# Kernel optimization log

Measured on AMD Instinct MI355X. Metric: run time of the kernel, lower is better.

## Reference

```python
import jax, jax.numpy as jnp
import numpy as np

THRESH_POSITIVE_AFFINITY = 0.65
THRESH_POSITIVE_REGION = 0.6
LAMBDA_WEIGHT = 2.0
TOPK_FALLBACK = 500


def _single_image_loss(pre_loss, label, thresh_positive):
    """Vectorized version of the per-sample pos/neg split + hard-negative top-k.

    pre_loss, label: [B, N] (flattened per-sample masked MSE maps / GT maps).
    Returns scalar sum over the batch of (pos_loss + neg_loss) per sample.
    """
    B, N = pre_loss.shape
    pos_mask = label > thresh_positive                      # [B, N] bool
    n_pos = jnp.sum(pos_mask, axis=-1)                      # [B] int
    n_neg = N - n_pos                                       # [B] int

    # positive loss: mean over positive pixels (0 if none)
    pos_sum = jnp.sum(jnp.where(pos_mask, pre_loss, 0.0), axis=-1)
    pos_loss = jnp.where(n_pos > 0, pos_sum / jnp.maximum(n_pos, 1), 0.0)

    # negatives sorted descending; positives pushed to the end via -inf
    neg_vals = jnp.where(pos_mask, -jnp.inf, pre_loss)
    sorted_neg = -jnp.sort(-neg_vals, axis=-1)              # [B, N] descending
    sorted_neg = jnp.where(jnp.isfinite(sorted_neg), sorted_neg, 0.0)
    csum = jnp.cumsum(sorted_neg, axis=-1)                  # [B, N]

    # k = 3*n_pos if enough negatives, else all negatives (torch branch)
    k = jnp.minimum(3 * n_pos, n_neg)                       # [B]
    k_idx = jnp.maximum(k - 1, 0)
    topk_sum = jnp.take_along_axis(csum, k_idx[:, None], axis=-1)[:, 0]
    neg_loss = jnp.where(k > 0, topk_sum / jnp.maximum(k, 1), 0.0)

    # fallback when no positives: mean of global top-500 of the loss map
    top500 = jnp.mean(jax.lax.top_k(pre_loss, TOPK_FALLBACK)[0], axis=-1)

    per_sample = jnp.where(n_pos > 0, pos_loss + neg_loss, top500)
    return jnp.sum(per_sample)


def setup_inputs() -> dict:
    key = jax.random.key(0)
    k1, k2, k3, k4, k5 = jax.random.split(key, 5)
    shape = (32, 512, 512)
    return {
        "region_score_gt": jax.random.uniform(k1, shape, dtype=jnp.float32),
        "affinity_score_gt": jax.random.uniform(k2, shape, dtype=jnp.float32),
        "region_score_pred": jax.random.normal(k3, shape, dtype=jnp.float32),
        "affinity_score_pred": jax.random.normal(k4, shape, dtype=jnp.float32),
        "mask": jax.random.uniform(k5, shape, dtype=jnp.float32),
    }


def reference(region_score_gt, affinity_score_gt, region_score_pred,
              affinity_score_pred, mask):
    # clamp predictions to 1 where GT is positive and pred overshoots 1
    rp = jnp.where((region_score_gt > THRESH_POSITIVE_REGION)
                   & (region_score_pred > 1.0), 1.0, region_score_pred)
    ap = jnp.where((affinity_score_gt > THRESH_POSITIVE_AFFINITY)
                   & (affinity_score_pred > 1.0), 1.0, affinity_score_pred)

    loss_g = (rp - region_score_gt) ** 2 * mask             # masked MSE map
    loss_a = (ap - affinity_score_gt) ** 2 * mask

    B = loss_g.shape[0]
    char_loss = _single_image_loss(loss_g.reshape(B, -1),
                                   region_score_gt.reshape(B, -1),
                                   THRESH_POSITIVE_REGION)
    affi_loss = _single_image_loss(loss_a.reshape(B, -1),
                                   affinity_score_gt.reshape(B, -1),
                                   THRESH_POSITIVE_AFFINITY)
    return LAMBDA_WEIGHT * char_loss / B + affi_loss / B
```

## Files before the change

kernel.cpp:

```cpp
#include <hip/hip_runtime.h>


#define NPS (512 * 512)
#define BPS 64
#define EPB 4096
#define NB 32

constexpr float THR_REGION = 0.6f;
constexpr float THR_AFF    = 0.65f;

__global__ __launch_bounds__(256) void map_loss_pass1(
    const float* __restrict__ rg, const float* __restrict__ ag,
    const float* __restrict__ rp, const float* __restrict__ ap,
    const float* __restrict__ mk, float* __restrict__ part) {
  const int b   = blockIdx.y;
  const int tid = threadIdx.x;
  const size_t sbase = (size_t)b * NPS + (size_t)blockIdx.x * EPB;

  float v[6] = {0.f, 0.f, 0.f, 0.f, 0.f, 0.f};

#pragma unroll
  for (int jj = 0; jj < 4; ++jj) {
    const size_t base = sbase + (size_t)jj * 1024 + (size_t)tid * 4;
    const float4 g_r = *reinterpret_cast<const float4*>(rg + base);
    const float4 g_a = *reinterpret_cast<const float4*>(ag + base);
    const float4 p_r = *reinterpret_cast<const float4*>(rp + base);
    const float4 p_a = *reinterpret_cast<const float4*>(ap + base);
    const float4 m_4 = *reinterpret_cast<const float4*>(mk + base);
    const float* gr = reinterpret_cast<const float*>(&g_r);
    const float* ga = reinterpret_cast<const float*>(&g_a);
    const float* pr = reinterpret_cast<const float*>(&p_r);
    const float* pa = reinterpret_cast<const float*>(&p_a);
    const float* mm = reinterpret_cast<const float*>(&m_4);
#pragma unroll
    for (int j = 0; j < 4; ++j) {
      const float m = mm[j];
      {
        const float g = gr[j];
        float p = pr[j];
        const bool pos = g > THR_REGION;
        if (pos && p > 1.0f) p = 1.0f;
        const float d = p - g;
        const float l = d * d * m;
        if (pos) { v[0] += l; v[2] += 1.0f; } else { v[1] += l; }
      }
      {
        const float g = ga[j];
        float p = pa[j];
        const bool pos = g > THR_AFF;
        if (pos && p > 1.0f) p = 1.0f;
        const float d = p - g;
        const float l = d * d * m;
        if (pos) { v[3] += l; v[5] += 1.0f; } else { v[4] += l; }
      }
    }
  }

#pragma unroll
  for (int q = 0; q < 6; ++q)
#pragma unroll
    for (int off = 32; off > 0; off >>= 1)
      v[q] += __shfl_down(v[q], off, 64);

  __shared__ float sh[4][6];
  const int lane = tid & 63, wid = tid >> 6;
  if (lane == 0) {
#pragma unroll
    for (int q = 0; q < 6; ++q) sh[wid][q] = v[q];
  }
  __syncthreads();
  if (tid < 6) {
    const float s = sh[0][tid] + sh[1][tid] + sh[2][tid] + sh[3][tid];
    part[((size_t)b * BPS + blockIdx.x) * 6 + tid] = s;
  }
}

__device__ float topk_sum_row(const float* __restrict__ gt,
                              const float* __restrict__ pd,
                              const float* __restrict__ mm,
                              float thr, int k, bool negOnly) {
  unsigned prefix = 0;
  float sum_def = 0.f;
  int want = k;
  for (int shift = 24; shift >= 0; shift -= 8) {
    unsigned cnt[256];
    float bsum[256];
    for (int i = 0; i < 256; ++i) { cnt[i] = 0; bsum[i] = 0.f; }
    for (int j = 0; j < NPS; ++j) {
      const float g = gt[j];
      const bool pos = g > thr;
      if (negOnly && pos) continue;
      float p = pd[j];
      if (pos && p > 1.0f) p = 1.0f;
      const float d = p - g;
      const float vv = d * d * mm[j];
      const unsigned u = __float_as_uint(vv);
      if (shift < 24 && (u >> (shift + 8)) != (prefix >> (shift + 8))) continue;
      const unsigned bin = (u >> shift) & 255u;
      cnt[bin]++;
      bsum[bin] += vv;
    }
    int bin = 255;
    for (; bin > 0; --bin) {
      if ((int)cnt[bin] < want) { want -= (int)cnt[bin]; sum_def += bsum[bin]; }
      else break;
    }
    prefix |= ((unsigned)bin) << shift;
  }
  sum_def += (float)want * __uint_as_float(prefix);
  return sum_def;
}

__global__ __launch_bounds__(64) void map_loss_pass2(
    const float* __restrict__ part,
    const float* __restrict__ rg, const float* __restrict__ ag,
    const float* __restrict__ rp, const float* __restrict__ ap,
    const float* __restrict__ mk, float* __restrict__ out) {
  const int t = threadIdx.x;
  const int mapA = t >> 5;
  const int b = t & 31;

  float posSum = 0.f, negSum = 0.f, cntF = 0.f;
  for (int blk = 0; blk < BPS; ++blk) {
    const float* p = part + ((size_t)b * BPS + blk) * 6 + mapA * 3;
    posSum += p[0];
    negSum += p[1];
    cntF   += p[2];
  }

  const int npos = (int)cntF;
  const int nneg = NPS - npos;
  long long k = 3LL * npos;
  if (k > nneg) k = nneg;

  const float thr = mapA ? THR_AFF : THR_REGION;
  const float* gt = (mapA ? ag : rg) + (size_t)b * NPS;
  const float* pd = (mapA ? ap : rp) + (size_t)b * NPS;
  const float* mm = mk + (size_t)b * NPS;

  float per_sample;
  if (npos > 0) {
    const float pos_loss = posSum / (float)npos;
    float neg_loss = 0.f;
    if (k > 0) {
      if (k == (long long)nneg) {
        neg_loss = negSum / (float)nneg;
      } else {
        neg_loss = topk_sum_row(gt, pd, mm, thr, (int)k, true) / (float)k;
      }
    }
    per_sample = pos_loss + neg_loss;
  } else {
    per_sample = topk_sum_row(gt, pd, mm, thr, 500, false) / 500.0f;
  }

  __shared__ float sh[64];
  sh[t] = per_sample;
  __syncthreads();
  if (t == 0) {
    float char_sum = 0.f, affi_sum = 0.f;
    for (int i = 0; i < 32; ++i) { char_sum += sh[i]; affi_sum += sh[32 + i]; }
    out[0] = 2.0f * char_sum / (float)NB + affi_sum / (float)NB;
  }
}

extern "C" void kernel_launch(void* const* d_in, const int* in_sizes, int n_in,
                              void* d_out, int out_size, void* d_ws, size_t ws_size,
                              hipStream_t stream) {
  const float* rg = (const float*)d_in[0];
  const float* ag = (const float*)d_in[1];
  const float* rp = (const float*)d_in[2];
  const float* ap = (const float*)d_in[3];
  const float* mk = (const float*)d_in[4];
  float* out = (float*)d_out;
  float* part = (float*)d_ws;

  dim3 grid1(BPS, NB);
  map_loss_pass1<<<grid1, 256, 0, stream>>>(rg, ag, rp, ap, mk, part);
  map_loss_pass2<<<1, 64, 0, stream>>>(part, rg, ag, rp, ap, mk, out);
}
```

Before: 34.47 us.

## Fuse partial reduction and finalization via last-block counter with cooperative top-k

Merges the two kernels into one: each block writes its partial sums, bumps an atomic counter, and the last block to finish does the per-sample finalization. The single-thread radix top-k is replaced by a 256-thread cooperative radix select using shared-memory histograms. This removes the separate tiny second kernel and its serial work, at the cost of an extra memset launch and atomic/threadfence overhead.

Result: slower. 106.2 us (+208.1%).

```diff
diff --git a/kernel.cpp b/kernel.cpp
--- a/kernel.cpp
+++ b/kernel.cpp
@@ -5,14 +5,81 @@
 #define BPS 64
 #define EPB 4096
 #define NB 32
+#define NBLK (BPS * NB)
 
 constexpr float THR_REGION = 0.6f;
 constexpr float THR_AFF    = 0.65f;
 
-__global__ __launch_bounds__(256) void map_loss_pass1(
+__device__ float coop_topk_sum(const float* __restrict__ gt,
+                               const float* __restrict__ pd,
+                               const float* __restrict__ mm,
+                               float thr, int k, bool negOnly, int tid) {
+  __shared__ unsigned hcnt[256];
+  __shared__ unsigned s_prefix;
+  __shared__ int s_want;
+  if (tid == 0) { s_prefix = 0; s_want = k; }
+  __syncthreads();
+  for (int shift = 24; shift >= 0; shift -= 8) {
+    hcnt[tid] = 0;
+    __syncthreads();
+    const unsigned pfx = s_prefix;
+    for (int j = tid; j < NPS; j += 256) {
+      const float g = gt[j];
+      const bool pos = g > thr;
+      if (negOnly && pos) continue;
+      float p = pd[j];
+      if (pos && p > 1.0f) p = 1.0f;
+      const float d = p - g;
+      const float vv = d * d * mm[j];
+      const unsigned u = __float_as_uint(vv);
+      if (shift < 24 && (u >> (shift + 8)) != (pfx >> (shift + 8))) continue;
+      atomicAdd(&hcnt[(u >> shift) & 255u], 1u);
+    }
+    __syncthreads();
+    if (tid == 0) {
+      int want = s_want;
+      int bin = 255;
+      for (; bin > 0; --bin) {
+        if ((int)hcnt[bin] < want) want -= (int)hcnt[bin];
+        else break;
+      }
+      s_want = want;
+      s_prefix |= ((unsigned)bin) << shift;
+    }
+    __syncthreads();
+  }
+  const unsigned T = s_prefix;
+  const int ties = s_want;
+  float psum = 0.f;
+  for (int j = tid; j < NPS; j += 256) {
+    const float g = gt[j];
+    const bool pos = g > thr;
+    if (negOnly && pos) continue;
+    float p = pd[j];
+    if (pos && p > 1.0f) p = 1.0f;
+    const float d = p - g;
+    const float vv = d * d * mm[j];
+    if (__float_as_uint(vv) > T) psum += vv;
+  }
+#pragma unroll
+  for (int off = 32; off; off >>= 1) psum += __shfl_down(psum, off, 64);
+  __shared__ float wsum[4];
+  if ((tid & 63) == 0) wsum[tid >> 6] = psum;
+  __syncthreads();
+  float total = 0.f;
+  if (tid == 0)
+    total = ((wsum[0] + wsum[1]) + (wsum[2] + wsum[3])) +
+            (float)ties * __uint_as_float(T);
+  __syncthreads();
+  return total;
+}
+
+__global__ __launch_bounds__(256) void map_loss_fused(
     const float* __restrict__ rg, const float* __restrict__ ag,
     const float* __restrict__ rp, const float* __restrict__ ap,
-    const float* __restrict__ mk, float* __restrict__ part) {
+    const float* __restrict__ mk,
+    unsigned* __restrict__ counter, float* __restrict__ part,
+    float* __restrict__ out) {
   const int b   = blockIdx.y;
   const int tid = threadIdx.x;
   const size_t sbase = (size_t)b * NPS + (size_t)blockIdx.x * EPB;
@@ -62,105 +129,93 @@
     for (int off = 32; off > 0; off >>= 1)
       v[q] += __shfl_down(v[q], off, 64);
 
-  __shared__ float sh[4][6];
+  __shared__ float shW[4][6];
   const int lane = tid & 63, wid = tid >> 6;
   if (lane == 0) {
 #pragma unroll
-    for (int q = 0; q < 6; ++q) sh[wid][q] = v[q];
-  }
-  __syncthreads();
-  if (tid < 6) {
-    const float s = sh[0][tid] + sh[1][tid] + sh[2][tid] + sh[3][tid];
-    part[((size_t)b * BPS + blockIdx.x) * 6 + tid] = s;
-  }
-}
-
-__device__ float topk_sum_row(const float* __restrict__ gt,
-                              const float* __restrict__ pd,
-                              const float* __restrict__ mm,
-                              float thr, int k, bool negOnly) {
-  unsigned prefix = 0;
-  float sum_def = 0.f;
-  int want = k;
-  for (int shift = 24; shift >= 0; shift -= 8) {
-    unsigned cnt[256];
-    float bsum[256];
-    for (int i = 0; i < 256; ++i) { cnt[i] = 0; bsum[i] = 0.f; }
-    for (int j = 0; j < NPS; ++j) {
-      const float g = gt[j];
-      const bool pos = g > thr;
-      if (negOnly && pos) continue;
-      float p = pd[j];
-      if (pos && p > 1.0f) p = 1.0f;
-      const float d = p - g;
-      const float vv = d * d * mm[j];
-      const unsigned u = __float_as_uint(vv);
-      if (shift < 24 && (u >> (shift + 8)) != (prefix >> (shift + 8))) continue;
-      const unsigned bin = (u >> shift) & 255u;
-      cnt[bin]++;
-      bsum[bin] += vv;
-    }
-    int bin = 255;
-    for (; bin > 0; --bin) {
-      if ((int)cnt[bin] < want) { want -= (int)cnt[bin]; sum_def += bsum[bin]; }
-      else break;
-    }
-    prefix |= ((unsigned)bin) << shift;
-  }
-  sum_def += (float)want * __uint_as_float(prefix);
-  return sum_def;
-}
-
-__global__ __launch_bounds__(64) void map_loss_pass2(
-    const float* __restrict__ part,
-    const float* __restrict__ rg, const float* __restrict__ ag,
-    const float* __restrict__ rp, const float* __restrict__ ap,
-    const float* __restrict__ mk, float* __restrict__ out) {
-  const int t = threadIdx.x;
-  const int mapA = t >> 5;
-  const int b = t & 31;
-
-  float posSum = 0.f, negSum = 0.f, cntF = 0.f;
-  for (int blk = 0; blk < BPS; ++blk) {
-    const float* p = part + ((size_t)b * BPS + blk) * 6 + mapA * 3;
-    posSum += p[0];
-    negSum += p[1];
-    cntF   += p[2];
-  }
-
-  const int npos = (int)cntF;
-  const int nneg = NPS - npos;
-  long long k = 3LL * npos;
-  if (k > nneg) k = nneg;
-
-  const float thr = mapA ? THR_AFF : THR_REGION;
-  const float* gt = (mapA ? ag : rg) + (size_t)b * NPS;
-  const float* pd = (mapA ? ap : rp) + (size_t)b * NPS;
-  const float* mm = mk + (size_t)b * NPS;
-
-  float per_sample;
-  if (npos > 0) {
-    const float pos_loss = posSum / (float)npos;
-    float neg_loss = 0.f;
-    if (k > 0) {
-      if (k == (long long)nneg) {
-        neg_loss = negSum / (float)nneg;
-      } else {
-        neg_loss = topk_sum_row(gt, pd, mm, thr, (int)k, true) / (float)k;
-      }
-    }
-    per_sample = pos_loss + neg_loss;
-  } else {
-    per_sample = topk_sum_row(gt, pd, mm, thr, 500, false) / 500.0f;
-  }
-
-  __shared__ float sh[64];
-  sh[t] = per_sample;
-  __syncthreads();
-  if (t == 0) {
-    float char_sum = 0.f, affi_sum = 0.f;
-    for (int i = 0; i < 32; ++i) { char_sum += sh[i]; affi_sum += sh[32 + i]; }
-    out[0] = 2.0f * char_sum / (float)NB + affi_sum / (float)NB;
+    for (int q = 0; q < 6; ++q) shW[wid][q] = v[q];
+  }
+  __syncthreads();
+
+  __shared__ int islast;
+  if (tid == 0) {
+    float* dst = part + ((size_t)b * BPS + blockIdx.x) * 6;
+#pragma unroll
+    for (int q = 0; q < 6; ++q)
+      dst[q] = shW[0][q] + shW[1][q] + shW[2][q] + shW[3][q];
+    __threadfence();
+    const unsigned tk = atomicAdd(counter, 1u);
+    islast = (tk == NBLK - 1) ? 1 : 0;
+  }
+  __syncthreads();
+  if (!islast) return;
+
+  __threadfence();
+
+  __shared__ float rsum[64][3];
+  {
+    const int row = tid >> 2, sub = tid & 3;
+    const int mapA = row >> 5, bb = row & 31;
+    float ps = 0.f, ns = 0.f, cf = 0.f;
+    for (int blk = sub; blk < BPS; blk += 4) {
+      const float* p = part + ((size_t)bb * BPS + blk) * 6 + mapA * 3;
+      ps += p[0]; ns += p[1]; cf += p[2];
+    }
+#pragma unroll
+    for (int m2 = 1; m2 <= 2; m2 <<= 1) {
+      ps += __shfl_xor(ps, m2, 64);
+      ns += __shfl_xor(ns, m2, 64);
+      cf += __shfl_xor(cf, m2, 64);
+    }
+    if (sub == 0) { rsum[row][0] = ps; rsum[row][1] = ns; rsum[row][2] = cf; }
+  }
+  __syncthreads();
+
+  __shared__ float per[64];
+  __shared__ int needK[64];
+  if (tid < 64) {
+    const int row = tid;
+    const int npos = (int)rsum[row][2];
+    const int nneg = NPS - npos;
+    long long k = 3LL * npos;
+    if (k > nneg) k = nneg;
+    float p_s = 0.f;
+    int nk = 0;
+    if (npos > 0) {
+      const float pos_loss = rsum[row][0] / (float)npos;
+      float neg_loss = 0.f;
+      if (k > 0) {
+        if (k == (long long)nneg) neg_loss = rsum[row][1] / (float)nneg;
+        else nk = (int)k;
+      }
+      p_s = pos_loss + neg_loss;
+    } else {
+      nk = -1;
+    }
+    per[row] = p_s;
+    needK[row] = nk;
+  }
+  __syncthreads();
+
+  for (int row = 0; row < 64; ++row) {
+    const int nk = needK[row];
+    if (nk == 0) continue;
+    const int mapA = row >> 5, bb = row & 31;
+    const float thr = mapA ? THR_AFF : THR_REGION;
+    const float* gt = (mapA ? ag : rg) + (size_t)bb * NPS;
+    const float* pd = (mapA ? ap : rp) + (size_t)bb * NPS;
+    const float* mm = mk + (size_t)bb * NPS;
+    const bool negOnly = (nk > 0);
+    const int k = negOnly ? nk : 500;
+    const float tsum = coop_topk_sum(gt, pd, mm, thr, k, negOnly, tid);
+    if (tid == 0) per[row] += tsum / (float)k;
+    __syncthreads();
+  }
+
+  if (tid == 0) {
+    float cs = 0.f, as_ = 0.f;
+    for (int i = 0; i < 32; ++i) { cs += per[i]; as_ += per[32 + i]; }
+    out[0] = 2.0f * cs / (float)NB + as_ / (float)NB;
   }
 }
 
@@ -173,9 +228,11 @@
   const float* ap = (const float*)d_in[3];
   const float* mk = (const float*)d_in[4];
   float* out = (float*)d_out;
-  float* part = (float*)d_ws;
-
-  dim3 grid1(BPS, NB);
-  map_loss_pass1<<<grid1, 256, 0, stream>>>(rg, ag, rp, ap, mk, part);
-  map_loss_pass2<<<1, 64, 0, stream>>>(part, rg, ag, rp, ap, mk, out);
+
+  unsigned* counter = (unsigned*)d_ws;
+  float* part = (float*)((char*)d_ws + 64);
+
+  hipMemsetAsync(counter, 0, sizeof(unsigned), stream);
+  dim3 grid(BPS, NB);
+  map_loss_fused<<<grid, 256, 0, stream>>>(rg, ag, rp, ap, mk, counter, part, out);
 }
```
